# Kernel optimization log

Measured on AMD Instinct MI355X. Metric: run time of the kernel, lower is better.

The kernel has to match this reference:

```python
import jax, jax.numpy as jnp
import numpy as np

D_MODEL = 1024
N_HEADS = 16
HEAD_DIM = 64
T = 4096
ROT = HEAD_DIM // 2          # 32 channels get rotary
PAIR = ROT // 2              # 16 cos/sin frequencies
EPS = 1e-6
SCALE = 0.12                 # constant attention scale (not 1/sqrt(d))
ROPE_BASE = 10000.0
VOCAB = 50257


def setup_inputs() -> dict:
    key = jax.random.key(0)
    k_x, k_qkv, k_o, k_tok = jax.random.split(key, 4)
    bound = 0.5 / np.sqrt(D_MODEL)
    x = jax.random.normal(k_x, (1, T, D_MODEL), dtype=jnp.float32)
    w_qkv = jax.random.uniform(k_qkv, (3 * D_MODEL, D_MODEL), jnp.float32, -bound, bound)
    # module uses zero_init for w_o; use small random so output is non-trivial
    w_o = jax.random.uniform(k_o, (D_MODEL, D_MODEL), jnp.float32, -bound, bound)
    q_norm_w = jnp.ones((HEAD_DIM,), jnp.float32)
    k_norm_w = jnp.ones((HEAD_DIM,), jnp.float32)
    tokens = jax.random.randint(k_tok, (1, T), 0, VOCAB, dtype=jnp.int64)
    pos = jnp.arange(T, dtype=jnp.int64)
    # RotaryCache: inv_freq over pair dims, cos/sin of t * inv_freq
    inv_freq = 1.0 / (ROPE_BASE ** (jnp.arange(PAIR, dtype=jnp.float32) / PAIR))
    freqs = jnp.arange(T, dtype=jnp.float32)[:, None] * inv_freq[None, :]  # [T, PAIR]
    return {
        "x": x, "tokens": tokens, "pos": pos,
        "w_qkv": w_qkv, "w_o": w_o,
        "q_norm_w": q_norm_w, "k_norm_w": k_norm_w,
        "cos": jnp.cos(freqs), "sin": jnp.sin(freqs),
        "window_tokens": 1024, "block_size": 128,
    }


def _rmsnorm(x, w):
    var = jnp.mean(x * x, axis=-1, keepdims=True)
    return x * jax.lax.rsqrt(var + EPS) * w


def reference(x, tokens, pos, w_qkv, w_o, q_norm_w, k_norm_w, cos, sin,
              window_tokens, block_size):
    B, Tq, C = x.shape
    H, Dh = N_HEADS, HEAD_DIM
    qkv = x @ w_qkv.T                                  # [B, T, 3C]
    q, k, v = jnp.split(qkv, 3, axis=-1)

    def to_bhtd(t):
        return t.reshape(B, Tq, H, Dh).transpose(0, 2, 1, 3)
    q, k, v = to_bhtd(q), to_bhtd(k), to_bhtd(v)

    q = _rmsnorm(q, q_norm_w)
    k = _rmsnorm(k, k_norm_w)

    # half-truncated RoPE: rotate first ROT channels pairwise (even/odd)
    c = cos[pos][None, None]                           # [1,1,T,PAIR]
    s = sin[pos][None, None]

    def rope_rotate(t):
        t1, t2 = t[..., :ROT], t[..., ROT:]
        even, odd = t1[..., 0::2], t1[..., 1::2]
        r_even = even * c - odd * s
        r_odd = even * s + odd * c
        t1r = jnp.stack([r_even, r_odd], axis=-1).reshape(t1.shape)
        return jnp.concatenate([t1r, t2], axis=-1)

    q = rope_rotate(q)
    k = rope_rotate(k)

    v = v * 0.5                                        # no value-embed branch

    scores = jnp.einsum('bhtd,bhsd->bhts', q, k) * SCALE
    idx = jnp.arange(Tq)
    diff = idx[:, None] - idx[None, :]
    allowed = (diff >= 0) & (diff < window_tokens)     # sliding causal window
    scores = jnp.where(allowed, scores, -jnp.inf)
    p = jax.nn.softmax(scores, axis=-1)
    out = jnp.einsum('bhts,bhsd->bhtd', p, v)
    out = out.transpose(0, 2, 1, 3).reshape(B, Tq, C)
    return out @ w_o.T
```

## Files before the change

### kernel.cpp

```cpp
#include <hip/hip_runtime.h>


typedef __bf16 bf16x8 __attribute__((ext_vector_type(8)));
typedef __bf16 bf16x2 __attribute__((ext_vector_type(2)));
typedef float f32x4 __attribute__((ext_vector_type(4)));
typedef unsigned short u16x8 __attribute__((ext_vector_type(8)));
typedef unsigned short u16x4 __attribute__((ext_vector_type(4)));

#define MFMA16(a, b, c) __builtin_amdgcn_mfma_f32_16x16x32_bf16((a), (b), (c), 0, 0, 0)

__device__ __forceinline__ unsigned short f2bf(float f) {
    unsigned int u = __float_as_uint(f);
    u += 0x7fffu + ((u >> 16) & 1u);
    return (unsigned short)(u >> 16);
}
__device__ __forceinline__ float bf2f(unsigned short h) {
    return __uint_as_float(((unsigned int)h) << 16);
}
__device__ __forceinline__ unsigned int pk2bf(float a, float b) {
#if __has_builtin(__builtin_amdgcn_cvt_pk_bf16_f32)
    bf16x2 v = __builtin_amdgcn_cvt_pk_bf16_f32(a, b);
    return __builtin_bit_cast(unsigned int, v);
#else
    return (unsigned int)f2bf(a) | ((unsigned int)f2bf(b) << 16);
#endif
}

__device__ __forceinline__ void gl_lds16(const void* g, void* l) {
    typedef __attribute__((address_space(1))) unsigned int GU;
    typedef __attribute__((address_space(3))) unsigned int LU;
    __builtin_amdgcn_global_load_lds((GU*)(unsigned long long)g,
                                     (LU*)(unsigned int)(unsigned long long)l,
                                     16, 0, 0);
}

__global__ void cvt3_kernel(const float* __restrict__ x,
                            const float* __restrict__ wqkv,
                            const float* __restrict__ wo,
                            unsigned short* __restrict__ xb,
                            unsigned short* __restrict__ wqkvb,
                            unsigned short* __restrict__ wob) {
    int i = blockIdx.x * 256 + threadIdx.x;
    const float* src;
    unsigned short* dst;
    int off;
    if (i < 1048576) { src = x; dst = xb; off = i; }
    else if (i < 1835008) { src = wqkv; dst = wqkvb; off = i - 1048576; }
    else { src = wo; dst = wob; off = i - 1835008; }
    float4 f = ((const float4*)src)[off];
    u16x4 o;
    o[0] = f2bf(f.x); o[1] = f2bf(f.y); o[2] = f2bf(f.z); o[3] = f2bf(f.w);
    ((u16x4*)dst)[off] = o;
}

__global__ __launch_bounds__(256) void gemm_qkv(
    const unsigned short* __restrict__ A,
    const unsigned short* __restrict__ Bt,
    const float* __restrict__ cosb, const float* __restrict__ sinb,
    const float* __restrict__ qw, const float* __restrict__ kw,
    unsigned short* __restrict__ Qb,
    unsigned short* __restrict__ Kb,
    unsigned short* __restrict__ Vt)
{
    __shared__ unsigned short As[128 * 32];
    __shared__ unsigned short Bs[128 * 32];
    __shared__ unsigned short tb[4][64 * 16];
    const int tid = threadIdx.x;
    const int wave = tid >> 6, lane = tid & 63;
    const int quad = lane >> 4, l16 = lane & 15;
    const int m0 = blockIdx.x * 128, n0 = blockIdx.y * 128;
    const int wm = (wave >> 1) * 64, wn = (wave & 1) * 64;
    (void)wn;

    f32x4 acc[4][4];
#pragma unroll
    for (int i = 0; i < 4; ++i)
#pragma unroll
        for (int j = 0; j < 4; ++j) acc[i][j] = (f32x4){0.f, 0.f, 0.f, 0.f};

    for (int k0 = 0; k0 < 1024; k0 += 32) {
#pragma unroll
        for (int i = 0; i < 2; ++i) {
            const int c = wave * 2 + i;
            const int e = (c * 64 + lane) * 8;
            const int r = e >> 5, col = e & 31;
            gl_lds16(A + (size_t)(m0 + r) * 1024 + (k0 + col), &As[c * 512]);
            gl_lds16(Bt + (size_t)(n0 + r) * 1024 + (k0 + col), &Bs[c * 512]);
        }
        __syncthreads();
        bf16x8 af[4], bfr[4];
#pragma unroll
        for (int mt = 0; mt < 4; ++mt)
            af[mt] = *(const bf16x8*)&As[(wm + mt * 16 + l16) * 32 + quad * 8];
#pragma unroll
        for (int nt = 0; nt < 4; ++nt)
            bfr[nt] = *(const bf16x8*)&Bs[((wave & 1) * 64 + nt * 16 + l16) * 32 + quad * 8];
#pragma unroll
        for (int mt = 0; mt < 4; ++mt)
#pragma unroll
            for (int nt = 0; nt < 4; ++nt)
                acc[mt][nt] = MFMA16(af[mt], bfr[nt], acc[mt][nt]);
        __syncthreads();
    }

    const int region = blockIdx.y >> 3;
    const int h = ((blockIdx.y & 7) << 1) + (wave & 1);

    if (region < 2) {
        const float* wgt = region ? kw : qw;
        unsigned short* dst = region ? Kb : Qb;
        float w[4];
#pragma unroll
        for (int nt = 0; nt < 4; ++nt) w[nt] = wgt[nt * 16 + l16];
#pragma unroll
        for (int mt = 0; mt < 4; ++mt)
#pragma unroll
            for (int r = 0; r < 4; ++r) {
                const int row = m0 + wm + mt * 16 + quad * 4 + r;
                float ss = 0.f;
#pragma unroll
                for (int nt = 0; nt < 4; ++nt)
                    ss += acc[mt][nt][r] * acc[mt][nt][r];
                ss += __shfl_xor(ss, 1); ss += __shfl_xor(ss, 2);
                ss += __shfl_xor(ss, 4); ss += __shfl_xor(ss, 8);
                const float rn = rsqrtf(ss * (1.f / 64.f) + 1e-6f);
                float val[4];
#pragma unroll
                for (int nt = 0; nt < 4; ++nt)
                    val[nt] = acc[mt][nt][r] * rn * w[nt];
#pragma unroll
                for (int nt = 0; nt < 2; ++nt) {
                    const float prt = __shfl_xor(val[nt], 1);
                    const int p = nt * 8 + (l16 >> 1);
                    const float c = cosb[row * 16 + p];
                    const float s = sinb[row * 16 + p];
                    val[nt] = (l16 & 1) ? (prt * s + val[nt] * c)
                                        : (val[nt] * c - prt * s);
                }
                const size_t ob = ((size_t)h * 4096 + row) * 64;
#pragma unroll
                for (int nt = 0; nt < 4; ++nt)
                    dst[ob + nt * 16 + l16] = f2bf(val[nt]);
            }
    } else {
        unsigned short* tbw = tb[wave];
#pragma unroll
        for (int mt = 0; mt < 4; ++mt) {
#pragma unroll
            for (int nt = 0; nt < 4; ++nt)
#pragma unroll
                for (int r = 0; r < 4; ++r)
                    tbw[(nt * 16 + l16) * 16 + quad * 4 + r] =
                        f2bf(acc[mt][nt][r] * 0.5f);
            u16x8 v0 = *(const u16x8*)&tbw[lane * 16];
            u16x8 v1 = *(const u16x8*)&tbw[lane * 16 + 8];
            const size_t vo = ((size_t)h * 64 + lane) * 4096 + m0 + wm + mt * 16;
            *(u16x8*)&Vt[vo] = v0;
            *(u16x8*)&Vt[vo + 8] = v1;
        }
    }
}

#define PSTR 72

template <int MODE>
__device__ __forceinline__ void attn_step(
    int s0, int tq, int wave, int quad, int l16, int krow, int kcol,
    const unsigned short* __restrict__ Kh, const unsigned short* __restrict__ Vh,
    unsigned short* Ks0, unsigned short* Ks1,
    unsigned short* Vs0, unsigned short* Vs1, unsigned short* Pw,
    const bf16x8 qf0, const bf16x8 qf1, f32x4 (&o)[4], float& lsum)
{
    __syncthreads();
    const unsigned short* kb = Kh + (size_t)(s0 + krow) * 64 + kcol;
    const unsigned short* vb = Vh + (size_t)krow * 4096 + s0 + kcol;
    gl_lds16(kb,      &Ks0[wave * 512]);
    gl_lds16(kb + 32, &Ks1[wave * 512]);
    gl_lds16(vb,      &Vs0[wave * 512]);
    gl_lds16(vb + 32, &Vs1[wave * 512]);
    __syncthreads();

    const float c = 0.17312340490667046f;
#pragma unroll
    for (int i = 0; i < 4; ++i) {
        const bf16x8 kf0 = *(const bf16x8*)&Ks0[(i * 16 + l16) * 32 + quad * 8];
        const bf16x8 kf1 = *(const bf16x8*)&Ks1[(i * 16 + l16) * 32 + quad * 8];
        f32x4 z = (f32x4){0.f, 0.f, 0.f, 0.f};
        z = MFMA16(kf0, qf0, z);
        z = MFMA16(kf1, qf1, z);
        float p[4];
#pragma unroll
        for (int r = 0; r < 4; ++r) {
            float e = exp2f(z[r] * c);
            if (MODE == 1) {
                const int s = s0 + i * 16 + quad * 4 + r;
                e = ((tq - s) < 1024) ? e : 0.f;
            }
            if (MODE == 2) {
                const int s = s0 + i * 16 + quad * 4 + r;
                e = (s <= tq) ? e : 0.f;
            }
            p[r] = e;
            lsum += e;
        }
        uint2 pk;
        pk.x = pk2bf(p[0], p[1]);
        pk.y = pk2bf(p[2], p[3]);
        *(uint2*)&Pw[l16 * PSTR + i * 16 + quad * 4] = pk;
    }
    const bf16x8 pf0 = *(const bf16x8*)&Pw[l16 * PSTR + quad * 8];
    const bf16x8 pf1 = *(const bf16x8*)&Pw[l16 * PSTR + 32 + quad * 8];
#pragma unroll
    for (int dt = 0; dt < 4; ++dt) {
        const bf16x8 vf0 = *(const bf16x8*)&Vs0[(dt * 16 + l16) * 32 + quad * 8];
        const bf16x8 vf1 = *(const bf16x8*)&Vs1[(dt * 16 + l16) * 32 + quad * 8];
        o[dt] = MFMA16(pf0, vf0, o[dt]);
        o[dt] = MFMA16(pf1, vf1, o[dt]);
    }
}

__global__ __launch_bounds__(256) void attn_kernel(
    const unsigned short* __restrict__ Qb,
    const unsigned short* __restrict__ Kb,
    const unsigned short* __restrict__ Vt,
    unsigned short* __restrict__ att)
{
    __shared__ unsigned short Ks0[64 * 32];
    __shared__ unsigned short Ks1[64 * 32];
    __shared__ unsigned short Vs0[64 * 32];
    __shared__ unsigned short Vs1[64 * 32];
    __shared__ unsigned short P[4][16 * PSTR];

    const int bid = blockIdx.x;
    const int h = ((bid & 7) << 1) | ((bid >> 3) & 1);
    const int t0 = (bid >> 4) * 64;

    const int tid = threadIdx.x;
    const int wave = tid >> 6, lane = tid & 63;
    const int quad = lane >> 4, l16 = lane & 15;
    const int qt0 = t0 + wave * 16;
    const int tq = qt0 + l16;
    const int krow = tid >> 2, kcol = (tid & 3) * 8;

    const unsigned short* Qh = Qb + (size_t)h * 4096 * 64;
    const unsigned short* Kh = Kb + (size_t)h * 4096 * 64;
    const unsigned short* Vh = Vt + (size_t)h * 64 * 4096;

    const bf16x8 qf0 = *(const bf16x8*)&Qh[(qt0 + l16) * 64 + quad * 8];
    const bf16x8 qf1 = *(const bf16x8*)&Qh[(qt0 + l16) * 64 + 32 + quad * 8];

    f32x4 o[4];
#pragma unroll
    for (int dt = 0; dt < 4; ++dt) o[dt] = (f32x4){0.f, 0.f, 0.f, 0.f};
    float lsum = 0.f;
    unsigned short* Pw = P[wave];

    int s0 = (t0 >= 1024) ? (t0 - 1024) : 0;
    if (t0 >= 1024) {
        attn_step<1>(s0, tq, wave, quad, l16, krow, kcol, Kh, Vh,
                     Ks0, Ks1, Vs0, Vs1, Pw, qf0, qf1, o, lsum);
        s0 += 64;
    }
    for (; s0 < t0; s0 += 64)
        attn_step<0>(s0, tq, wave, quad, l16, krow, kcol, Kh, Vh,
                     Ks0, Ks1, Vs0, Vs1, Pw, qf0, qf1, o, lsum);
    attn_step<2>(t0, tq, wave, quad, l16, krow, kcol, Kh, Vh,
                 Ks0, Ks1, Vs0, Vs1, Pw, qf0, qf1, o, lsum);

    lsum += __shfl_xor(lsum, 16);
    lsum += __shfl_xor(lsum, 32);
    float lr[4];
#pragma unroll
    for (int r = 0; r < 4; ++r) lr[r] = 1.f / __shfl(lsum, quad * 4 + r);
#pragma unroll
    for (int dt = 0; dt < 4; ++dt)
#pragma unroll
        for (int r = 0; r < 4; ++r)
            att[(size_t)(qt0 + quad * 4 + r) * 1024 + h * 64 + dt * 16 + l16] =
                f2bf(o[dt][r] * lr[r]);
}

template <int BM, bool F32OUT>
__global__ __launch_bounds__(256) void gemm_bt(
    const unsigned short* __restrict__ A,
    const unsigned short* __restrict__ Bt,
    void* __restrict__ Cp, int N, int K) {
    __shared__ unsigned short As[BM * 32];
    __shared__ unsigned short Bs[128 * 32];
    constexpr int MT = BM / 32;
    const int tid = threadIdx.x;
    const int wave = tid >> 6, lane = tid & 63;
    const int quad = lane >> 4, l16 = lane & 15;
    const int m0 = blockIdx.x * BM, n0 = blockIdx.y * 128;
    const int wm = (wave >> 1) * (BM / 2), wn = (wave & 1) * 64;

    f32x4 acc[MT][4];
#pragma unroll
    for (int i = 0; i < MT; ++i)
#pragma unroll
        for (int j = 0; j < 4; ++j) acc[i][j] = (f32x4){0.f, 0.f, 0.f, 0.f};

    for (int k0 = 0; k0 < K; k0 += 32) {
#pragma unroll
        for (int i = 0; i < BM / 64; ++i) {
            const int c = wave * (BM / 64) + i;
            const int e = (c * 64 + lane) * 8;
            const int r = e >> 5, col = e & 31;
            gl_lds16(A + (size_t)(m0 + r) * K + (k0 + col), &As[c * 512]);
        }
#pragma unroll
        for (int i = 0; i < 2; ++i) {
            const int c = wave * 2 + i;
            const int e = (c * 64 + lane) * 8;
            const int r = e >> 5, col = e & 31;
            gl_lds16(Bt + (size_t)(n0 + r) * K + (k0 + col), &Bs[c * 512]);
        }
        __syncthreads();
        bf16x8 af[MT], bfr[4];
#pragma unroll
        for (int mt = 0; mt < MT; ++mt)
            af[mt] = *(const bf16x8*)&As[(wm + mt * 16 + l16) * 32 + quad * 8];
#pragma unroll
        for (int nt = 0; nt < 4; ++nt)
            bfr[nt] = *(const bf16x8*)&Bs[(wn + nt * 16 + l16) * 32 + quad * 8];
#pragma unroll
        for (int mt = 0; mt < MT; ++mt)
#pragma unroll
            for (int nt = 0; nt < 4; ++nt)
                acc[mt][nt] = MFMA16(af[mt], bfr[nt], acc[mt][nt]);
        __syncthreads();
    }
#pragma unroll
    for (int mt = 0; mt < MT; ++mt)
#pragma unroll
        for (int nt = 0; nt < 4; ++nt)
#pragma unroll
            for (int r = 0; r < 4; ++r) {
                const int row = m0 + wm + mt * 16 + quad * 4 + r;
                const int col = n0 + wn + nt * 16 + l16;
                const float v = acc[mt][nt][r];
                if (F32OUT)
                    ((float*)Cp)[(size_t)row * N + col] = v;
                else
                    ((unsigned short*)Cp)[(size_t)row * N + col] = f2bf(v);
            }
}

extern "C" void kernel_launch(void* const* d_in, const int* in_sizes, int n_in,
                              void* d_out, int out_size, void* d_ws, size_t ws_size,
                              hipStream_t stream) {
    const float* x    = (const float*)d_in[0];
    const float* wqkv = (const float*)d_in[3];
    const float* wo   = (const float*)d_in[4];
    const float* qw   = (const float*)d_in[5];
    const float* kw   = (const float*)d_in[6];
    const float* cosb = (const float*)d_in[7];
    const float* sinb = (const float*)d_in[8];

    char* ws = (char*)d_ws;
    if (ws_size < (size_t)48 * 1024 * 1024) return;
    unsigned short* xb    = (unsigned short*)(ws + ((size_t)0 << 20));
    unsigned short* wqkvb = (unsigned short*)(ws + ((size_t)8 << 20));
    unsigned short* wob   = (unsigned short*)(ws + ((size_t)14 << 20));
    unsigned short* Qb    = (unsigned short*)(ws + ((size_t)16 << 20));
    unsigned short* Kb    = (unsigned short*)(ws + ((size_t)24 << 20));
    unsigned short* Vt    = (unsigned short*)(ws + ((size_t)32 << 20));
    unsigned short* attb  = (unsigned short*)(ws + ((size_t)40 << 20));

    cvt3_kernel<<<8192, 256, 0, stream>>>(x, wqkv, wo, xb, wqkvb, wob);

    gemm_qkv<<<dim3(32, 24), 256, 0, stream>>>(xb, wqkvb, cosb, sinb, qw, kw,
                                               Qb, Kb, Vt);

    attn_kernel<<<1024, 256, 0, stream>>>(Qb, Kb, Vt, attb);

    gemm_bt<64, true><<<dim3(64, 8), 256, 0, stream>>>(attb, wob, (float*)d_out, 1024, 1024);
}
```

Before: 209.0 us.

## Double-buffer LDS staging in GEMMs and attention; vectorize Q/K stores

Adds ping-pong shared-memory buffers to the QKV GEMM, output GEMM and attention kernel, so the next tile's global-to-LDS loads are issued before computing on the current tile. This drops one barrier per iteration and lets memory latency overlap with MFMA work. The Q/K epilogue now goes through a padded LDS transpose buffer and writes 16-byte vectors instead of scalar 2-byte stores. LDS use per block doubles, which may lower occupancy. It also relies on the gl_lds16 writes being complete at the single remaining barrier.

```diff
diff --git a/kernel.cpp b/kernel.cpp
--- a/kernel.cpp
+++ b/kernel.cpp
@@ -53,6 +53,7 @@
     ((u16x4*)dst)[off] = o;
 }
 
+#define TBS 72
 __global__ __launch_bounds__(256) void gemm_qkv(
     const unsigned short* __restrict__ A,
     const unsigned short* __restrict__ Bt,
@@ -62,15 +63,14 @@
     unsigned short* __restrict__ Kb,
     unsigned short* __restrict__ Vt)
 {
-    __shared__ unsigned short As[128 * 32];
-    __shared__ unsigned short Bs[128 * 32];
-    __shared__ unsigned short tb[4][64 * 16];
+    __shared__ unsigned short As[2][128 * 32];
+    __shared__ unsigned short Bs[2][128 * 32];
+    __shared__ unsigned short tb[4][16 * TBS];
     const int tid = threadIdx.x;
     const int wave = tid >> 6, lane = tid & 63;
     const int quad = lane >> 4, l16 = lane & 15;
     const int m0 = blockIdx.x * 128, n0 = blockIdx.y * 128;
-    const int wm = (wave >> 1) * 64, wn = (wave & 1) * 64;
-    (void)wn;
+    const int wm = (wave >> 1) * 64;
 
     f32x4 acc[4][4];
 #pragma unroll
@@ -78,33 +78,41 @@
 #pragma unroll
         for (int j = 0; j < 4; ++j) acc[i][j] = (f32x4){0.f, 0.f, 0.f, 0.f};
 
-    for (int k0 = 0; k0 < 1024; k0 += 32) {
+    auto stageAB = [&](int buf, int k0) {
 #pragma unroll
         for (int i = 0; i < 2; ++i) {
             const int c = wave * 2 + i;
             const int e = (c * 64 + lane) * 8;
             const int r = e >> 5, col = e & 31;
-            gl_lds16(A + (size_t)(m0 + r) * 1024 + (k0 + col), &As[c * 512]);
-            gl_lds16(Bt + (size_t)(n0 + r) * 1024 + (k0 + col), &Bs[c * 512]);
-        }
-        __syncthreads();
+            gl_lds16(A + (size_t)(m0 + r) * 1024 + (k0 + col), &As[buf][c * 512]);
+            gl_lds16(Bt + (size_t)(n0 + r) * 1024 + (k0 + col), &Bs[buf][c * 512]);
+        }
+    };
+
+    stageAB(0, 0);
+    __syncthreads();
+    int buf = 0;
+    for (int k0 = 0; k0 < 1024; k0 += 32) {
+        if (k0 + 32 < 1024) stageAB(buf ^ 1, k0 + 32);
         bf16x8 af[4], bfr[4];
 #pragma unroll
         for (int mt = 0; mt < 4; ++mt)
-            af[mt] = *(const bf16x8*)&As[(wm + mt * 16 + l16) * 32 + quad * 8];
+            af[mt] = *(const bf16x8*)&As[buf][(wm + mt * 16 + l16) * 32 + quad * 8];
 #pragma unroll
         for (int nt = 0; nt < 4; ++nt)
-            bfr[nt] = *(const bf16x8*)&Bs[((wave & 1) * 64 + nt * 16 + l16) * 32 + quad * 8];
+            bfr[nt] = *(const bf16x8*)&Bs[buf][((wave & 1) * 64 + nt * 16 + l16) * 32 + quad * 8];
 #pragma unroll
         for (int mt = 0; mt < 4; ++mt)
 #pragma unroll
             for (int nt = 0; nt < 4; ++nt)
                 acc[mt][nt] = MFMA16(af[mt], bfr[nt], acc[mt][nt]);
         __syncthreads();
+        buf ^= 1;
     }
 
     const int region = blockIdx.y >> 3;
     const int h = ((blockIdx.y & 7) << 1) + (wave & 1);
+    unsigned short* tbw = tb[wave];
 
     if (region < 2) {
         const float* wgt = region ? kw : qw;
@@ -113,7 +121,7 @@
 #pragma unroll
         for (int nt = 0; nt < 4; ++nt) w[nt] = wgt[nt * 16 + l16];
 #pragma unroll
-        for (int mt = 0; mt < 4; ++mt)
+        for (int mt = 0; mt < 4; ++mt) {
 #pragma unroll
             for (int r = 0; r < 4; ++r) {
                 const int row = m0 + wm + mt * 16 + quad * 4 + r;
@@ -137,13 +145,18 @@
                     val[nt] = (l16 & 1) ? (prt * s + val[nt] * c)
                                         : (val[nt] * c - prt * s);
                 }
-                const size_t ob = ((size_t)h * 4096 + row) * 64;
 #pragma unroll
                 for (int nt = 0; nt < 4; ++nt)
-                    dst[ob + nt * 16 + l16] = f2bf(val[nt]);
+                    tbw[(quad * 4 + r) * TBS + nt * 16 + l16] = f2bf(val[nt]);
             }
+            const int t = lane >> 2, dcol = (lane & 3) * 16;
+            u16x8 v0 = *(const u16x8*)&tbw[t * TBS + dcol];
+            u16x8 v1 = *(const u16x8*)&tbw[t * TBS + dcol + 8];
+            const size_t ob = ((size_t)h * 4096 + (m0 + wm + mt * 16 + t)) * 64 + dcol;
+            *(u16x8*)&dst[ob] = v0;
+            *(u16x8*)&dst[ob + 8] = v1;
+        }
     } else {
-        unsigned short* tbw = tb[wave];
 #pragma unroll
         for (int mt = 0; mt < 4; ++mt) {
 #pragma unroll
@@ -164,22 +177,13 @@
 #define PSTR 72
 
 template <int MODE>
-__device__ __forceinline__ void attn_step(
-    int s0, int tq, int wave, int quad, int l16, int krow, int kcol,
-    const unsigned short* __restrict__ Kh, const unsigned short* __restrict__ Vh,
-    unsigned short* Ks0, unsigned short* Ks1,
-    unsigned short* Vs0, unsigned short* Vs1, unsigned short* Pw,
+__device__ __forceinline__ void attn_compute(
+    int s0, int tq, int quad, int l16,
+    const unsigned short* Ks0, const unsigned short* Ks1,
+    const unsigned short* Vs0, const unsigned short* Vs1,
+    unsigned short* Pw,
     const bf16x8 qf0, const bf16x8 qf1, f32x4 (&o)[4], float& lsum)
 {
-    __syncthreads();
-    const unsigned short* kb = Kh + (size_t)(s0 + krow) * 64 + kcol;
-    const unsigned short* vb = Vh + (size_t)krow * 4096 + s0 + kcol;
-    gl_lds16(kb,      &Ks0[wave * 512]);
-    gl_lds16(kb + 32, &Ks1[wave * 512]);
-    gl_lds16(vb,      &Vs0[wave * 512]);
-    gl_lds16(vb + 32, &Vs1[wave * 512]);
-    __syncthreads();
-
     const float c = 0.17312340490667046f;
 #pragma unroll
     for (int i = 0; i < 4; ++i) {
@@ -225,10 +229,10 @@
     const unsigned short* __restrict__ Vt,
     unsigned short* __restrict__ att)
 {
-    __shared__ unsigned short Ks0[64 * 32];
-    __shared__ unsigned short Ks1[64 * 32];
-    __shared__ unsigned short Vs0[64 * 32];
-    __shared__ unsigned short Vs1[64 * 32];
+    __shared__ unsigned short Ks0[2][64 * 32];
+    __shared__ unsigned short Ks1[2][64 * 32];
+    __shared__ unsigned short Vs0[2][64 * 32];
+    __shared__ unsigned short Vs1[2][64 * 32];
     __shared__ unsigned short P[4][16 * PSTR];
 
     const int bid = blockIdx.x;
@@ -255,17 +259,33 @@
     float lsum = 0.f;
     unsigned short* Pw = P[wave];
 
-    int s0 = (t0 >= 1024) ? (t0 - 1024) : 0;
-    if (t0 >= 1024) {
-        attn_step<1>(s0, tq, wave, quad, l16, krow, kcol, Kh, Vh,
-                     Ks0, Ks1, Vs0, Vs1, Pw, qf0, qf1, o, lsum);
-        s0 += 64;
-    }
-    for (; s0 < t0; s0 += 64)
-        attn_step<0>(s0, tq, wave, quad, l16, krow, kcol, Kh, Vh,
-                     Ks0, Ks1, Vs0, Vs1, Pw, qf0, qf1, o, lsum);
-    attn_step<2>(t0, tq, wave, quad, l16, krow, kcol, Kh, Vh,
-                 Ks0, Ks1, Vs0, Vs1, Pw, qf0, qf1, o, lsum);
+    auto stage = [&](int buf, int s0) {
+        const unsigned short* kb = Kh + (size_t)(s0 + krow) * 64 + kcol;
+        const unsigned short* vb = Vh + (size_t)krow * 4096 + s0 + kcol;
+        gl_lds16(kb,      &Ks0[buf][wave * 512]);
+        gl_lds16(kb + 32, &Ks1[buf][wave * 512]);
+        gl_lds16(vb,      &Vs0[buf][wave * 512]);
+        gl_lds16(vb + 32, &Vs1[buf][wave * 512]);
+    };
+
+    const int sbase = (t0 >= 1024) ? (t0 - 1024) : 0;
+    stage(0, sbase);
+    __syncthreads();
+    int buf = 0;
+    for (int s0 = sbase; s0 <= t0; s0 += 64) {
+        if (s0 + 64 <= t0) stage(buf ^ 1, s0 + 64);
+        if (s0 == sbase && t0 >= 1024)
+            attn_compute<1>(s0, tq, quad, l16, Ks0[buf], Ks1[buf], Vs0[buf],
+                            Vs1[buf], Pw, qf0, qf1, o, lsum);
+        else if (s0 == t0)
+            attn_compute<2>(s0, tq, quad, l16, Ks0[buf], Ks1[buf], Vs0[buf],
+                            Vs1[buf], Pw, qf0, qf1, o, lsum);
+        else
+            attn_compute<0>(s0, tq, quad, l16, Ks0[buf], Ks1[buf], Vs0[buf],
+                            Vs1[buf], Pw, qf0, qf1, o, lsum);
+        __syncthreads();
+        buf ^= 1;
+    }
 
     lsum += __shfl_xor(lsum, 16);
     lsum += __shfl_xor(lsum, 32);
@@ -285,8 +305,8 @@
     const unsigned short* __restrict__ A,
     const unsigned short* __restrict__ Bt,
     void* __restrict__ Cp, int N, int K) {
-    __shared__ unsigned short As[BM * 32];
-    __shared__ unsigned short Bs[128 * 32];
+    __shared__ unsigned short As[2][BM * 32];
+    __shared__ unsigned short Bs[2][128 * 32];
     constexpr int MT = BM / 32;
     const int tid = threadIdx.x;
     const int wave = tid >> 6, lane = tid & 63;
@@ -300,35 +320,42 @@
 #pragma unroll
         for (int j = 0; j < 4; ++j) acc[i][j] = (f32x4){0.f, 0.f, 0.f, 0.f};
 
-    for (int k0 = 0; k0 < K; k0 += 32) {
+    auto stageAB = [&](int buf, int k0) {
 #pragma unroll
         for (int i = 0; i < BM / 64; ++i) {
             const int c = wave * (BM / 64) + i;
             const int e = (c * 64 + lane) * 8;
             const int r = e >> 5, col = e & 31;
-            gl_lds16(A + (size_t)(m0 + r) * K + (k0 + col), &As[c * 512]);
+            gl_lds16(A + (size_t)(m0 + r) * K + (k0 + col), &As[buf][c * 512]);
         }
 #pragma unroll
         for (int i = 0; i < 2; ++i) {
             const int c = wave * 2 + i;
             const int e = (c * 64 + lane) * 8;
             const int r = e >> 5, col = e & 31;
-            gl_lds16(Bt + (size_t)(n0 + r) * K + (k0 + col), &Bs[c * 512]);
-        }
-        __syncthreads();
+            gl_lds16(Bt + (size_t)(n0 + r) * K + (k0 + col), &Bs[buf][c * 512]);
+        }
+    };
+
+    stageAB(0, 0);
+    __syncthreads();
+    int buf = 0;
+    for (int k0 = 0; k0 < K; k0 += 32) {
+        if (k0 + 32 < K) stageAB(buf ^ 1, k0 + 32);
         bf16x8 af[MT], bfr[4];
 #pragma unroll
         for (int mt = 0; mt < MT; ++mt)
-            af[mt] = *(const bf16x8*)&As[(wm + mt * 16 + l16) * 32 + quad * 8];
+            af[mt] = *(const bf16x8*)&As[buf][(wm + mt * 16 + l16) * 32 + quad * 8];
 #pragma unroll
         for (int nt = 0; nt < 4; ++nt)
-            bfr[nt] = *(const bf16x8*)&Bs[(wn + nt * 16 + l16) * 32 + quad * 8];
+            bfr[nt] = *(const bf16x8*)&Bs[buf][(wn + nt * 16 + l16) * 32 + quad * 8];
 #pragma unroll
         for (int mt = 0; mt < MT; ++mt)
 #pragma unroll
             for (int nt = 0; nt < 4; ++nt)
                 acc[mt][nt] = MFMA16(af[mt], bfr[nt], acc[mt][nt]);
         __syncthreads();
+        buf ^= 1;
     }
 #pragma unroll
     for (int mt = 0; mt < MT; ++mt)
```

New measurement: 192.5 us. -7.9%, faster.
